# Kernel optimization log

Hardware: AMD Instinct MI355X
Metric: run time of the kernel (lower is better)

The kernel has to match this reference:

```python
import jax, jax.numpy as jnp
import numpy as np

B, T, S = 1, 8, 1024
HID, H = 1152, 16
D = HID // H  # 72
EPS = 1e-6


def rmsnorm(t, gamma):
    # t: [b,t,s,h,d], gamma: [h,d] per-head learnable scale (QKNorm)
    var = jnp.mean(jnp.square(t), axis=-1, keepdims=True)
    return t * jax.lax.rsqrt(var + EPS) * gamma


def setup_inputs() -> dict:
    key = jax.random.key(0)
    ks = jax.random.split(key, 8)
    sc = lambda fan_in: 1.0 / np.sqrt(fan_in)
    x = jax.random.normal(ks[0], (B, T, S, HID), dtype=jnp.float32)
    Wq = jax.random.normal(ks[1], (HID, HID), dtype=jnp.float32) * sc(HID)
    bq = jnp.zeros((HID,), dtype=jnp.float32)
    Wkv = jax.random.normal(ks[2], (HID, 2 * HID), dtype=jnp.float32) * sc(HID)
    bkv = jnp.zeros((2 * HID,), dtype=jnp.float32)
    q_gamma = jnp.ones((H, D), dtype=jnp.float32)
    k_gamma = jnp.ones((H, D), dtype=jnp.float32)
    Wo = jax.random.normal(ks[3], (HID, HID), dtype=jnp.float32) * sc(HID)
    return {"x": x, "Wq": Wq, "bq": bq, "Wkv": Wkv, "bkv": bkv,
            "q_gamma": q_gamma, "k_gamma": k_gamma, "Wo": Wo}


def reference(x, Wq, bq, Wkv, bkv, q_gamma, k_gamma, Wo):
    b, t, s, _ = x.shape
    q = (x @ Wq + bq).reshape(b, t, s, H, D)
    kv = x @ Wkv + bkv
    k, v = jnp.split(kv, 2, axis=-1)
    k = k.reshape(b, t, s, H, D)
    v = v.reshape(b, t, s, H, D)
    q = rmsnorm(q, q_gamma)
    k = rmsnorm(k, k_gamma)
    # NOTE: original applies no 1/sqrt(d) scaling (QKNorm replaces it)
    attn_weight = jnp.einsum('btqhd,btkhd->bthqk', q, k)
    attn = jax.nn.softmax(attn_weight, axis=-1)
    out = jnp.einsum('bthqk,btkhd->btqhd', attn, v).reshape(b, t, s, HID)
    return out @ Wo
```

## Files before the change

### kernel.cpp

```cpp
#include <hip/hip_runtime.h>


typedef __attribute__((ext_vector_type(4))) short s16x4;
typedef __attribute__((ext_vector_type(8))) short s16x8;
typedef __attribute__((ext_vector_type(4))) float f32x4;
typedef __attribute__((ext_vector_type(16))) float f32x16;

__device__ __forceinline__ unsigned short f2b(float x) {
  unsigned u = __float_as_uint(x);
  u += 0x7FFFu + ((u >> 16) & 1u);
  return (unsigned short)(u >> 16);
}
__device__ __forceinline__ float b2f(unsigned short u) {
  return __uint_as_float(((unsigned)u) << 16);
}
__device__ __forceinline__ void gld16(const void* g, void* l) {
  __builtin_amdgcn_global_load_lds(
      (const __attribute__((address_space(1))) void*)g,
      (__attribute__((address_space(3))) void*)l, 16, 0, 0);
}

__global__ __launch_bounds__(256) void cvt_bf16_kernel(const float* __restrict__ in,
                                                       unsigned short* __restrict__ out,
                                                       int n16) {
  int i = blockIdx.x * 256 + threadIdx.x;
  if (i >= n16) return;
  const float4* p = (const float4*)(in + (size_t)i * 16);
  float4 a = p[0], b = p[1], c = p[2], d = p[3];
  s16x8 r0, r1;
  r0[0] = (short)f2b(a.x); r0[1] = (short)f2b(a.y); r0[2] = (short)f2b(a.z); r0[3] = (short)f2b(a.w);
  r0[4] = (short)f2b(c.x); r0[5] = (short)f2b(c.y); r0[6] = (short)f2b(c.z); r0[7] = (short)f2b(c.w);
  r1[0] = (short)f2b(b.x); r1[1] = (short)f2b(b.y); r1[2] = (short)f2b(b.z); r1[3] = (short)f2b(b.w);
  r1[4] = (short)f2b(d.x); r1[5] = (short)f2b(d.y); r1[6] = (short)f2b(d.z); r1[7] = (short)f2b(d.w);
  *(s16x8*)(out + (size_t)i * 16) = r0;
  *(s16x8*)(out + (size_t)i * 16 + 8) = r1;
}

__global__ __launch_bounds__(256) void transpose_cvt_kernel(const float* __restrict__ W,
                                                            unsigned short* __restrict__ WT,
                                                            int K, int N) {
  __shared__ float tile[32][33];
  int n0 = blockIdx.x * 32, k0 = blockIdx.y * 32;
  int tx = threadIdx.x, ty = threadIdx.y;
#pragma unroll
  for (int i = 0; i < 4; i++)
    tile[ty + i * 8][tx] = W[(size_t)(k0 + ty + i * 8) * N + n0 + tx];
  __syncthreads();
  int stx = (tx & 19) | ((tx & 4) << 1) | ((tx & 8) >> 1);
#pragma unroll
  for (int i = 0; i < 4; i++)
    WT[(size_t)(n0 + ty + i * 8) * K + k0 + stx] = f2b(tile[tx][ty + i * 8]);
}

__global__ __launch_bounds__(256) void gemm_qkv_kernel(const unsigned short* __restrict__ A,
                                                       const unsigned short* __restrict__ BT,
                                                       const float* __restrict__ biasq,
                                                       const float* __restrict__ biaskv,
                                                       unsigned short* __restrict__ qn,
                                                       unsigned short* __restrict__ kn,
                                                       unsigned short* __restrict__ vt) {
  constexpr int K = 1152;
  constexpr int NT = K / 32;
  __shared__ __align__(16) unsigned short As[3 * 8192];
  __shared__ __align__(16) unsigned short Bs[3 * 4096];
  int tid = threadIdx.x;
  int lane = tid & 63, wave = tid >> 6;
  int wr = (wave >> 1) * 128, wc = (wave & 1) * 64;
  int l31 = lane & 31, lh = lane >> 5;
  int bid = blockIdx.x;
  int xcd = bid & 7;
  int w = bid >> 3;
  int st = w / 12, inner = w - st * 12;
  int ibx = inner % 3, iby = inner / 3;
  int bx = st * 3 + ibx;
  int by = xcd * 4 + iby;
  int brow = by * 256, bcol = bx * 128;
  const unsigned short* AsrcP[4];
  const unsigned short* BsrcP[2];
  int dstA[4], dstB[2];
#pragma unroll
  for (int i = 0; i < 4; i++) {
    int c = tid + 256 * i;
    int row = c >> 2, j = c & 3;
    AsrcP[i] = A + (size_t)(brow + row) * K + (j ^ ((row >> 1) & 3)) * 8;
    dstA[i] = (wave * 64 + 256 * i) * 8;
  }
#pragma unroll
  for (int i = 0; i < 2; i++) {
    int c = tid + 256 * i;
    int row = c >> 2, j = c & 3;
    BsrcP[i] = BT + (size_t)(bcol + row) * K + (j ^ ((row >> 1) & 3)) * 8;
    dstB[i] = (wave * 64 + 256 * i) * 8;
  }
#define STAGE(KT, BUF)                                           \
  {                                                              \
    int kb = (KT) * 32;                                          \
    gld16(AsrcP[0] + kb, &As[(BUF) * 8192 + dstA[0]]);           \
    gld16(AsrcP[1] + kb, &As[(BUF) * 8192 + dstA[1]]);           \
    gld16(AsrcP[2] + kb, &As[(BUF) * 8192 + dstA[2]]);           \
    gld16(AsrcP[3] + kb, &As[(BUF) * 8192 + dstA[3]]);           \
    gld16(BsrcP[0] + kb, &Bs[(BUF) * 4096 + dstB[0]]);           \
    gld16(BsrcP[1] + kb, &Bs[(BUF) * 4096 + dstB[1]]);           \
  }
  int fr = (l31 >> 1) & 3;
  int slotk[2] = {(lh ^ fr) * 8, ((2 + lh) ^ fr) * 8};
  STAGE(0, 0);
  STAGE(1, 1);
  f32x16 acc[4][2] = {};
  int cur = 0;
  for (int kt = 0; kt < NT; kt++) {
    if (kt < NT - 1)
      asm volatile("s_waitcnt vmcnt(6)\n\ts_barrier" ::: "memory");
    else
      asm volatile("s_waitcnt vmcnt(0)\n\ts_barrier" ::: "memory");
    if (kt + 2 < NT) {
      int nb = (cur == 0) ? 2 : cur - 1;
      STAGE(kt + 2, nb);
    }
    int ab = cur * 8192, bb = cur * 4096;
#pragma unroll
    for (int kk = 0; kk < 2; kk++) {
      int so = slotk[kk];
      s16x8 af[4], bf[2];
#pragma unroll
      for (int m = 0; m < 4; m++)
        af[m] = *(const s16x8*)&As[ab + (wr + m * 32 + l31) * 32 + so];
#pragma unroll
      for (int n = 0; n < 2; n++)
        bf[n] = *(const s16x8*)&Bs[bb + (wc + n * 32 + l31) * 32 + so];
      __builtin_amdgcn_s_setprio(1);
#pragma unroll
      for (int m = 0; m < 4; m++)
#pragma unroll
        for (int n = 0; n < 2; n++)
          acc[m][n] = __builtin_amdgcn_mfma_f32_32x32x16_bf16(af[m], bf[n], acc[m][n], 0, 0, 0);
      __builtin_amdgcn_s_setprio(0);
    }
    cur = (cur == 2) ? 0 : cur + 1;
  }
#undef STAGE
#pragma unroll
  for (int m = 0; m < 4; m++) {
#pragma unroll
    for (int n = 0; n < 2; n++) {
#pragma unroll
      for (int reg = 0; reg < 16; reg++) {
        int grow = brow + wr + m * 32 + (reg & 3) + 8 * (reg >> 2) + 4 * lh;
        int gcol = bcol + wc + n * 32 + l31;
        float v = acc[m][n][reg];
        v += (gcol < 1152) ? biasq[gcol] : biaskv[gcol - 1152];
        int t = grow >> 10, s = grow & 1023;
        if (gcol < 2304) {
          int c = (gcol < 1152) ? gcol : gcol - 1152;
          int h = c / 72, d = c - h * 72;
          unsigned short* dst = (gcol < 1152) ? qn : kn;
          dst[((size_t)((t * 16 + h) * 1024 + s)) * 96 + d] = f2b(v);
        } else {
          int c = gcol - 2304;
          int h = c / 72, d = c - h * 72;
          vt[((size_t)((t * 16 + h) * 80 + d)) * 1024 + s] = f2b(v);
        }
      }
    }
  }
}

__global__ __launch_bounds__(256) void gemm_out_kernel(const unsigned short* __restrict__ A,
                                                       const unsigned short* __restrict__ BT,
                                                       int N, int gx,
                                                       float* __restrict__ outF) {
  constexpr int K = 1152;
  constexpr int NT = K / 32;
  __shared__ __align__(16) unsigned short As[3 * 4096];
  __shared__ __align__(16) unsigned short Bs[3 * 4096];
  int tid = threadIdx.x;
  int lane = tid & 63, wave = tid >> 6;
  int wr = (wave >> 1) * 64, wc = (wave & 1) * 64;
  int l31 = lane & 31, lh = lane >> 5;
  int bid = blockIdx.x;
  int xcd = bid & 7;
  int w = bid >> 3;
  int st = w / 24, inner = w - st * 24;
  int ibx = inner % 3, iby = inner / 3;
  int bx = st * 3 + ibx;
  int by = xcd * 8 + iby;
  int brow = by * 128, bcol = bx * 128;
  const unsigned short* AsrcP[2];
  const unsigned short* BsrcP[2];
  int dst0[2];
#pragma unroll
  for (int i = 0; i < 2; i++) {
    int c = tid + 256 * i;
    int row = c >> 2, j = c & 3;
    int ch = j ^ ((row >> 1) & 3);
    AsrcP[i] = A + (size_t)(brow + row) * K + ch * 8;
    BsrcP[i] = BT + (size_t)(bcol + row) * K + ch * 8;
    dst0[i] = (wave * 64 + 256 * i) * 8;
  }
#define STAGE(KT, BUF)                                          \
  {                                                             \
    int kb = (KT) * 32;                                         \
    gld16(AsrcP[0] + kb, &As[(BUF) * 4096 + dst0[0]]);          \
    gld16(BsrcP[0] + kb, &Bs[(BUF) * 4096 + dst0[0]]);          \
    gld16(AsrcP[1] + kb, &As[(BUF) * 4096 + dst0[1]]);          \
    gld16(BsrcP[1] + kb, &Bs[(BUF) * 4096 + dst0[1]]);          \
  }
  int fr = (l31 >> 1) & 3;
  int slotk[2] = {(lh ^ fr) * 8, ((2 + lh) ^ fr) * 8};
  STAGE(0, 0);
  STAGE(1, 1);
  f32x16 acc[2][2] = {};
  int cur = 0;
  for (int kt = 0; kt < NT; kt++) {
    if (kt < NT - 1)
      asm volatile("s_waitcnt vmcnt(4)\n\ts_barrier" ::: "memory");
    else
      asm volatile("s_waitcnt vmcnt(0)\n\ts_barrier" ::: "memory");
    if (kt + 2 < NT) {
      int nb = (cur == 0) ? 2 : cur - 1;
      STAGE(kt + 2, nb);
    }
    int ab = cur * 4096;
#pragma unroll
    for (int kk = 0; kk < 2; kk++) {
      int so = slotk[kk];
      s16x8 af[2], bf[2];
#pragma unroll
      for (int m = 0; m < 2; m++)
        af[m] = *(const s16x8*)&As[ab + (wr + m * 32 + l31) * 32 + so];
#pragma unroll
      for (int n = 0; n < 2; n++)
        bf[n] = *(const s16x8*)&Bs[ab + (wc + n * 32 + l31) * 32 + so];
      __builtin_amdgcn_s_setprio(1);
#pragma unroll
      for (int m = 0; m < 2; m++)
#pragma unroll
        for (int n = 0; n < 2; n++)
          acc[m][n] = __builtin_amdgcn_mfma_f32_32x32x16_bf16(af[m], bf[n], acc[m][n], 0, 0, 0);
      __builtin_amdgcn_s_setprio(0);
    }
    cur = (cur == 2) ? 0 : cur + 1;
  }
#undef STAGE
#pragma unroll
  for (int m = 0; m < 2; m++) {
#pragma unroll
    for (int n = 0; n < 2; n++) {
#pragma unroll
      for (int reg = 0; reg < 16; reg++) {
        int grow = brow + wr + m * 32 + (reg & 3) + 8 * (reg >> 2) + 4 * lh;
        int gcol = bcol + wc + n * 32 + l31;
        outF[(size_t)grow * N + gcol] = acc[m][n][reg];
      }
    }
  }
}

__global__ __launch_bounds__(256) void rmsnorm2_kernel(unsigned short* __restrict__ qn,
                                                       unsigned short* __restrict__ kn,
                                                       const float* __restrict__ qg,
                                                       const float* __restrict__ kg) {
  int r = blockIdx.x * 4 + (threadIdx.x >> 6);
  int isK = r >= 131072;
  int g = isK ? r - 131072 : r;
  unsigned short* buf = isK ? kn : qn;
  const float* gamma = isK ? kg : qg;
  int h = (g >> 10) & 15;
  size_t base = (size_t)g * 96;
  int l = threadIdx.x & 63;
  float e0 = b2f(buf[base + l]);
  float e1 = 0.f;
  if (l < 8) e1 = b2f(buf[base + 64 + l]);
  float ss = e0 * e0 + e1 * e1;
#pragma unroll
  for (int m = 1; m < 64; m <<= 1) ss += __shfl_xor(ss, m);
  float sc = rsqrtf(ss * (1.0f / 72.0f) + 1e-6f);
  buf[base + l] = f2b(e0 * sc * gamma[h * 72 + l]);
  if (l < 32) {
    float v = 0.f;
    if (l < 8) v = e1 * sc * gamma[h * 72 + 64 + l];
    buf[base + 64 + l] = f2b(v);
  }
}

__global__ __launch_bounds__(256) void attn_kernel(const unsigned short* __restrict__ Qn,
                                                   const unsigned short* __restrict__ Kn,
                                                   const unsigned short* __restrict__ VtG,
                                                   unsigned short* __restrict__ att) {
  __shared__ unsigned short Kl[2][64][100];
  __shared__ unsigned short Vt[2][80][76];
  int tid = threadIdx.x;
  int lane = tid & 63, wave = tid >> 6;
  int l15 = lane & 15, lq = lane >> 4, kf = lq * 4;
  int bid = blockIdx.x;
  int orig = (bid & 7) * 128 + (bid >> 3);
  int qb = orig & 7, th = orig >> 3;
  int t = th >> 4, h = th & 15;
  const unsigned short* Q = Qn + (size_t)th * 1024 * 96;
  const unsigned short* Kp = Kn + (size_t)th * 1024 * 96;
  const unsigned short* Vg = VtG + (size_t)th * 80 * 1024;
  int qrow0 = qb * 128 + wave * 32;
  int krow[3], kco[3], vd[3], vco[3];
#pragma unroll
  for (int i = 0; i < 3; i++) {
    int c = tid + i * 256;
    krow[i] = c / 12;
    kco[i] = c - 12 * krow[i];
    int cc = tid + i * 256;
    vd[i] = cc >> 3;
    vco[i] = cc & 7;
  }
  bool v2 = tid < 128;
  s16x8 sk[3], sv[3];
  s16x8 qf[2][3];
#pragma unroll
  for (int g = 0; g < 2; g++)
#pragma unroll
    for (int c = 0; c < 3; c++) {
      const unsigned short* p = Q + (size_t)(qrow0 + g * 16 + l15) * 96 + c * 32 + kf;
      s16x4 lo = *(const s16x4*)p;
      s16x4 hi = *(const s16x4*)(p + 16);
      qf[g][c] = __builtin_shufflevector(lo, hi, 0, 1, 2, 3, 4, 5, 6, 7);
    }
  f32x4 o[2][5] = {};
  float m_r[2] = {-3.0e38f, -3.0e38f}, l_r[2] = {0.f, 0.f};

#pragma unroll
  for (int i = 0; i < 3; i++)
    sk[i] = *(const s16x8*)(Kp + (size_t)krow[i] * 96 + kco[i] * 8);
#pragma unroll
  for (int i = 0; i < 2; i++)
    sv[i] = *(const s16x8*)(Vg + (size_t)vd[i] * 1024 + vco[i] * 8);
  if (v2) sv[2] = *(const s16x8*)(Vg + (size_t)vd[2] * 1024 + vco[2] * 8);
#pragma unroll
  for (int i = 0; i < 3; i++) *(s16x8*)&Kl[0][krow[i]][kco[i] * 8] = sk[i];
#pragma unroll
  for (int i = 0; i < 2; i++) *(s16x8*)&Vt[0][vd[i]][vco[i] * 8] = sv[i];
  if (v2) *(s16x8*)&Vt[0][vd[2]][vco[2] * 8] = sv[2];

  for (int tt = 0; tt < 16; tt++) {
    __syncthreads();
    int cur = tt & 1;
    if (tt < 15) {
      int kv1 = (tt + 1) * 64;
#pragma unroll
      for (int i = 0; i < 3; i++)
        sk[i] = *(const s16x8*)(Kp + (size_t)(kv1 + krow[i]) * 96 + kco[i] * 8);
#pragma unroll
      for (int i = 0; i < 2; i++)
        sv[i] = *(const s16x8*)(Vg + (size_t)vd[i] * 1024 + kv1 + vco[i] * 8);
      if (v2) sv[2] = *(const s16x8*)(Vg + (size_t)vd[2] * 1024 + kv1 + vco[2] * 8);
    }
#pragma unroll
    for (int g = 0; g < 2; g++) {
      f32x4 st[4];
      __builtin_amdgcn_s_setprio(1);
#pragma unroll
      for (int n = 0; n < 4; n++) {
        f32x4 a = {};
#pragma unroll
        for (int c = 0; c < 3; c++) {
          s16x4 lo = *(const s16x4*)&Kl[cur][n * 16 + l15][c * 32 + kf];
          s16x4 hi = *(const s16x4*)&Kl[cur][n * 16 + l15][c * 32 + kf + 16];
          s16x8 kfr = __builtin_shufflevector(lo, hi, 0, 1, 2, 3, 4, 5, 6, 7);
          a = __builtin_amdgcn_mfma_f32_16x16x32_bf16(kfr, qf[g][c], a, 0, 0, 0);
        }
        st[n] = a;
      }
      __builtin_amdgcn_s_setprio(0);
      float tmax = st[0][0];
#pragma unroll
      for (int n = 0; n < 4; n++)
#pragma unroll
        for (int r = 0; r < 4; r++) tmax = fmaxf(tmax, st[n][r]);
      tmax = fmaxf(tmax, __shfl_xor(tmax, 16));
      tmax = fmaxf(tmax, __shfl_xor(tmax, 32));
      float mn = fmaxf(m_r[g], tmax);
      float scale = __expf(m_r[g] - mn);
      m_r[g] = mn;
      float sum = 0.f;
#pragma unroll
      for (int n = 0; n < 4; n++)
#pragma unroll
        for (int r = 0; r < 4; r++) {
          float p = __expf(st[n][r] - mn);
          st[n][r] = p;
          sum += p;
        }
      sum += __shfl_xor(sum, 16);
      sum += __shfl_xor(sum, 32);
      l_r[g] = l_r[g] * scale + sum;
#pragma unroll
      for (int r = 0; r < 4; r++) {
        float scq = __shfl(scale, 4 * lq + r);
#pragma unroll
        for (int v = 0; v < 5; v++) o[g][v][r] *= scq;
      }
      __builtin_amdgcn_s_setprio(1);
#pragma unroll
      for (int b = 0; b < 2; b++) {
        s16x8 pf;
#pragma unroll
        for (int j = 0; j < 8; j++) pf[j] = (short)f2b(st[2 * b + (j >> 2)][j & 3]);
#pragma unroll
        for (int v = 0; v < 5; v++) {
          s16x4 vlo = *(const s16x4*)&Vt[cur][v * 16 + l15][b * 32 + kf];
          s16x4 vhi = *(const s16x4*)&Vt[cur][v * 16 + l15][b * 32 + kf + 16];
          s16x8 vf = __builtin_shufflevector(vlo, vhi, 0, 1, 2, 3, 4, 5, 6, 7);
          o[g][v] = __builtin_amdgcn_mfma_f32_16x16x32_bf16(pf, vf, o[g][v], 0, 0, 0);
        }
      }
      __builtin_amdgcn_s_setprio(0);
    }
    if (tt < 15) {
      int nxt = cur ^ 1;
#pragma unroll
      for (int i = 0; i < 3; i++) *(s16x8*)&Kl[nxt][krow[i]][kco[i] * 8] = sk[i];
#pragma unroll
      for (int i = 0; i < 2; i++) *(s16x8*)&Vt[nxt][vd[i]][vco[i] * 8] = sv[i];
      if (v2) *(s16x8*)&Vt[nxt][vd[2]][vco[2] * 8] = sv[2];
    }
  }
#pragma unroll
  for (int g = 0; g < 2; g++)
#pragma unroll
    for (int r = 0; r < 4; r++) {
      float inv = 1.0f / __shfl(l_r[g], 4 * lq + r);
      int qrow = qrow0 + g * 16 + 4 * lq + r;
      size_t rowbase = (size_t)(t * 1024 + qrow) * 1152;
#pragma unroll
      for (int v = 0; v < 5; v++) {
        int d = v * 16 + l15;
        if (d < 72) {
          int col = h * 72 + d;
          int scol = (col & ~12) | ((col & 4) << 1) | ((col & 8) >> 1);
          att[rowbase + scol] = f2b(o[g][v][r] * inv);
        }
      }
    }
}

extern "C" void kernel_launch(void* const* d_in, const int* in_sizes, int n_in,
                              void* d_out, int out_size, void* d_ws, size_t ws_size,
                              hipStream_t stream) {
  const float* x   = (const float*)d_in[0];
  const float* Wq  = (const float*)d_in[1];
  const float* bq  = (const float*)d_in[2];
  const float* Wkv = (const float*)d_in[3];
  const float* bkv = (const float*)d_in[4];
  const float* qg  = (const float*)d_in[5];
  const float* kg  = (const float*)d_in[6];
  const float* Wo  = (const float*)d_in[7];
  float* out = (float*)d_out;

  char* w = (char*)d_ws;
  unsigned short* xb   = (unsigned short*)w; w += (size_t)8192 * 1152 * 2;
  unsigned short* WqT  = (unsigned short*)w; w += (size_t)1152 * 1152 * 2;
  unsigned short* WkvT = (unsigned short*)w; w += (size_t)2304 * 1152 * 2;
  unsigned short* WoT  = (unsigned short*)w; w += (size_t)1152 * 1152 * 2;
  unsigned short* qn   = (unsigned short*)w; w += (size_t)128 * 1024 * 96 * 2;
  unsigned short* kn   = (unsigned short*)w; w += (size_t)128 * 1024 * 96 * 2;
  unsigned short* vt   = (unsigned short*)w; w += (size_t)128 * 80 * 1024 * 2;
  unsigned short* att  = (unsigned short*)w; w += (size_t)8192 * 1152 * 2;

  cvt_bf16_kernel<<<2304, 256, 0, stream>>>(x, xb, 9437184 / 16);
  transpose_cvt_kernel<<<dim3(36, 36), dim3(32, 8), 0, stream>>>(Wq, WqT, 1152, 1152);
  transpose_cvt_kernel<<<dim3(72, 36), dim3(32, 8), 0, stream>>>(Wkv, WkvT, 1152, 2304);
  transpose_cvt_kernel<<<dim3(36, 36), dim3(32, 8), 0, stream>>>(Wo, WoT, 1152, 1152);

  gemm_qkv_kernel<<<864, 256, 0, stream>>>(xb, WqT, bq, bkv, qn, kn, vt);
  rmsnorm2_kernel<<<65536, 256, 0, stream>>>(qn, kn, qg, kg);

  attn_kernel<<<1024, 256, 0, stream>>>(qn, kn, vt, att);

  gemm_out_kernel<<<576, 256, 0, stream>>>(att, WoT, 1152, 9, out);
}
```

Measured before the change: 308.8 us.

## Stage V-transpose epilogue through LDS and share K fragments across query groups

In the QKV GEMM, blocks producing V columns now write the biased bf16 tile transposed into shared memory, then emit 16-byte coalesced stores to the transposed V layout instead of scattered 2-byte stores. Bias and head-index math are hoisted out of the per-register loop for Q/K. In attention, the two query groups now share each K fragment read from LDS, issuing both QK MFMAs per load, which halves K LDS reads but keeps both score tiles live and raises register pressure.

```diff
diff --git a/kernel.cpp b/kernel.cpp
--- a/kernel.cpp
+++ b/kernel.cpp
@@ -61,8 +61,9 @@
                                                        unsigned short* __restrict__ vt) {
   constexpr int K = 1152;
   constexpr int NT = K / 32;
-  __shared__ __align__(16) unsigned short As[3 * 8192];
-  __shared__ __align__(16) unsigned short Bs[3 * 4096];
+  __shared__ __align__(16) unsigned short LDSU[3 * 8192 + 3 * 4096];
+  unsigned short* As = LDSU;
+  unsigned short* Bs = LDSU + 3 * 8192;
   int tid = threadIdx.x;
   int lane = tid & 63, wave = tid >> 6;
   int wr = (wave >> 1) * 128, wc = (wave & 1) * 64;
@@ -139,26 +140,49 @@
     cur = (cur == 2) ? 0 : cur + 1;
   }
 #undef STAGE
-#pragma unroll
-  for (int m = 0; m < 4; m++) {
-#pragma unroll
-    for (int n = 0; n < 2; n++) {
-#pragma unroll
-      for (int reg = 0; reg < 16; reg++) {
-        int grow = brow + wr + m * 32 + (reg & 3) + 8 * (reg >> 2) + 4 * lh;
+  if (bcol >= 2304) {
+    __syncthreads();
+    int c0 = bcol - 2304;
+#pragma unroll
+    for (int m = 0; m < 4; m++) {
+#pragma unroll
+      for (int n = 0; n < 2; n++) {
+        int col = wc + n * 32 + l31;
+        float bias = biaskv[1152 + c0 + col];
+#pragma unroll
+        for (int reg = 0; reg < 16; reg++) {
+          int row = wr + m * 32 + (reg & 3) + 8 * (reg >> 2) + 4 * lh;
+          LDSU[col * 264 + row] = f2b(acc[m][n][reg] + bias);
+        }
+      }
+    }
+    __syncthreads();
+    int t = brow >> 10, sbase = brow & 1023;
+#pragma unroll
+    for (int i = 0; i < 16; i++) {
+      int id = tid + 256 * i;
+      int col = id >> 5, rowc = id & 31;
+      int c = c0 + col;
+      int h = c / 72, d = c - h * 72;
+      s16x8 v8 = *(const s16x8*)&LDSU[col * 264 + rowc * 8];
+      *(s16x8*)(vt + ((size_t)((t * 16 + h) * 80 + d)) * 1024 + sbase + rowc * 8) = v8;
+    }
+  } else {
+#pragma unroll
+    for (int m = 0; m < 4; m++) {
+#pragma unroll
+      for (int n = 0; n < 2; n++) {
         int gcol = bcol + wc + n * 32 + l31;
-        float v = acc[m][n][reg];
-        v += (gcol < 1152) ? biasq[gcol] : biaskv[gcol - 1152];
-        int t = grow >> 10, s = grow & 1023;
-        if (gcol < 2304) {
-          int c = (gcol < 1152) ? gcol : gcol - 1152;
-          int h = c / 72, d = c - h * 72;
-          unsigned short* dst = (gcol < 1152) ? qn : kn;
+        float bias = (gcol < 1152) ? biasq[gcol] : biaskv[gcol - 1152];
+        int c = (gcol < 1152) ? gcol : gcol - 1152;
+        int h = c / 72, d = c - h * 72;
+        unsigned short* dst = (gcol < 1152) ? qn : kn;
+#pragma unroll
+        for (int reg = 0; reg < 16; reg++) {
+          int grow = brow + wr + m * 32 + (reg & 3) + 8 * (reg >> 2) + 4 * lh;
+          float v = acc[m][n][reg] + bias;
+          int t = grow >> 10, s = grow & 1023;
           dst[((size_t)((t * 16 + h) * 1024 + s)) * 96 + d] = f2b(v);
-        } else {
-          int c = gcol - 2304;
-          int h = c / 72, d = c - h * 72;
-          vt[((size_t)((t * 16 + h) * 80 + d)) * 1024 + s] = f2b(v);
         }
       }
     }
@@ -312,16 +336,18 @@
   }
   bool v2 = tid < 128;
   s16x8 sk[3], sv[3];
-  s16x8 qf[2][3];
-#pragma unroll
-  for (int g = 0; g < 2; g++)
-#pragma unroll
-    for (int c = 0; c < 3; c++) {
-      const unsigned short* p = Q + (size_t)(qrow0 + g * 16 + l15) * 96 + c * 32 + kf;
-      s16x4 lo = *(const s16x4*)p;
-      s16x4 hi = *(const s16x4*)(p + 16);
-      qf[g][c] = __builtin_shufflevector(lo, hi, 0, 1, 2, 3, 4, 5, 6, 7);
-    }
+  s16x8 qf0[3], qf1[3];
+#pragma unroll
+  for (int c = 0; c < 3; c++) {
+    const unsigned short* p0 = Q + (size_t)(qrow0 + l15) * 96 + c * 32 + kf;
+    s16x4 lo = *(const s16x4*)p0;
+    s16x4 hi = *(const s16x4*)(p0 + 16);
+    qf0[c] = __builtin_shufflevector(lo, hi, 0, 1, 2, 3, 4, 5, 6, 7);
+    const unsigned short* p1 = Q + (size_t)(qrow0 + 16 + l15) * 96 + c * 32 + kf;
+    s16x4 lo1 = *(const s16x4*)p1;
+    s16x4 hi1 = *(const s16x4*)(p1 + 16);
+    qf1[c] = __builtin_shufflevector(lo1, hi1, 0, 1, 2, 3, 4, 5, 6, 7);
+  }
   f32x4 o[2][5] = {};
   float m_r[2] = {-3.0e38f, -3.0e38f}, l_r[2] = {0.f, 0.f};
 
@@ -351,67 +377,71 @@
         sv[i] = *(const s16x8*)(Vg + (size_t)vd[i] * 1024 + kv1 + vco[i] * 8);
       if (v2) sv[2] = *(const s16x8*)(Vg + (size_t)vd[2] * 1024 + kv1 + vco[2] * 8);
     }
-#pragma unroll
-    for (int g = 0; g < 2; g++) {
-      f32x4 st[4];
-      __builtin_amdgcn_s_setprio(1);
-#pragma unroll
-      for (int n = 0; n < 4; n++) {
-        f32x4 a = {};
-#pragma unroll
-        for (int c = 0; c < 3; c++) {
-          s16x4 lo = *(const s16x4*)&Kl[cur][n * 16 + l15][c * 32 + kf];
-          s16x4 hi = *(const s16x4*)&Kl[cur][n * 16 + l15][c * 32 + kf + 16];
-          s16x8 kfr = __builtin_shufflevector(lo, hi, 0, 1, 2, 3, 4, 5, 6, 7);
-          a = __builtin_amdgcn_mfma_f32_16x16x32_bf16(kfr, qf[g][c], a, 0, 0, 0);
-        }
-        st[n] = a;
+    f32x4 st0[4], st1[4];
+    __builtin_amdgcn_s_setprio(1);
+#pragma unroll
+    for (int n = 0; n < 4; n++) {
+      f32x4 a0 = {}, a1 = {};
+#pragma unroll
+      for (int c = 0; c < 3; c++) {
+        s16x4 lo = *(const s16x4*)&Kl[cur][n * 16 + l15][c * 32 + kf];
+        s16x4 hi = *(const s16x4*)&Kl[cur][n * 16 + l15][c * 32 + kf + 16];
+        s16x8 kfr = __builtin_shufflevector(lo, hi, 0, 1, 2, 3, 4, 5, 6, 7);
+        a0 = __builtin_amdgcn_mfma_f32_16x16x32_bf16(kfr, qf0[c], a0, 0, 0, 0);
+        a1 = __builtin_amdgcn_mfma_f32_16x16x32_bf16(kfr, qf1[c], a1, 0, 0, 0);
       }
-      __builtin_amdgcn_s_setprio(0);
-      float tmax = st[0][0];
-#pragma unroll
-      for (int n = 0; n < 4; n++)
-#pragma unroll
-        for (int r = 0; r < 4; r++) tmax = fmaxf(tmax, st[n][r]);
-      tmax = fmaxf(tmax, __shfl_xor(tmax, 16));
-      tmax = fmaxf(tmax, __shfl_xor(tmax, 32));
-      float mn = fmaxf(m_r[g], tmax);
-      float scale = __expf(m_r[g] - mn);
-      m_r[g] = mn;
-      float sum = 0.f;
-#pragma unroll
-      for (int n = 0; n < 4; n++)
-#pragma unroll
-        for (int r = 0; r < 4; r++) {
-          float p = __expf(st[n][r] - mn);
-          st[n][r] = p;
-          sum += p;
-        }
-      sum += __shfl_xor(sum, 16);
-      sum += __shfl_xor(sum, 32);
-      l_r[g] = l_r[g] * scale + sum;
-#pragma unroll
-      for (int r = 0; r < 4; r++) {
-        float scq = __shfl(scale, 4 * lq + r);
-#pragma unroll
-        for (int v = 0; v < 5; v++) o[g][v][r] *= scq;
-      }
-      __builtin_amdgcn_s_setprio(1);
-#pragma unroll
-      for (int b = 0; b < 2; b++) {
-        s16x8 pf;
-#pragma unroll
-        for (int j = 0; j < 8; j++) pf[j] = (short)f2b(st[2 * b + (j >> 2)][j & 3]);
-#pragma unroll
-        for (int v = 0; v < 5; v++) {
-          s16x4 vlo = *(const s16x4*)&Vt[cur][v * 16 + l15][b * 32 + kf];
-          s16x4 vhi = *(const s16x4*)&Vt[cur][v * 16 + l15][b * 32 + kf + 16];
-          s16x8 vf = __builtin_shufflevector(vlo, vhi, 0, 1, 2, 3, 4, 5, 6, 7);
-          o[g][v] = __builtin_amdgcn_mfma_f32_16x16x32_bf16(pf, vf, o[g][v], 0, 0, 0);
-        }
-      }
-      __builtin_amdgcn_s_setprio(0);
-    }
+      st0[n] = a0;
+      st1[n] = a1;
+    }
+    __builtin_amdgcn_s_setprio(0);
+#define SOFTMAX(ST, G)                                                        \
+    {                                                                         \
+      float tmax = ST[0][0];                                                  \
+      _Pragma("unroll") for (int n = 0; n < 4; n++)                           \
+        _Pragma("unroll") for (int r = 0; r < 4; r++)                         \
+          tmax = fmaxf(tmax, ST[n][r]);                                       \
+      tmax = fmaxf(tmax, __shfl_xor(tmax, 16));                               \
+      tmax = fmaxf(tmax, __shfl_xor(tmax, 32));                               \
+      float mn = fmaxf(m_r[G], tmax);                                         \
+      float scale = __expf(m_r[G] - mn);                                      \
+      m_r[G] = mn;                                                            \
+      float sum = 0.f;                                                        \
+      _Pragma("unroll") for (int n = 0; n < 4; n++)                           \
+        _Pragma("unroll") for (int r = 0; r < 4; r++) {                       \
+          float p = __expf(ST[n][r] - mn);                                    \
+          ST[n][r] = p;                                                       \
+          sum += p;                                                           \
+        }                                                                     \
+      sum += __shfl_xor(sum, 16);                                             \
+      sum += __shfl_xor(sum, 32);                                             \
+      l_r[G] = l_r[G] * scale + sum;                                          \
+      _Pragma("unroll") for (int r = 0; r < 4; r++) {                         \
+        float scq = __shfl(scale, 4 * lq + r);                                \
+        _Pragma("unroll") for (int v = 0; v < 5; v++) o[G][v][r] *= scq;      \
+      }                                                                       \
+    }
+#define PV(ST, G)                                                             \
+    {                                                                         \
+      __builtin_amdgcn_s_setprio(1);                                          \
+      _Pragma("unroll") for (int b = 0; b < 2; b++) {                         \
+        s16x8 pf;                                                             \
+        _Pragma("unroll") for (int j = 0; j < 8; j++)                         \
+          pf[j] = (short)f2b(ST[2 * b + (j >> 2)][j & 3]);                    \
+        _Pragma("unroll") for (int v = 0; v < 5; v++) {                       \
+          s16x4 vlo = *(const s16x4*)&Vt[cur][v * 16 + l15][b * 32 + kf];     \
+          s16x4 vhi = *(const s16x4*)&Vt[cur][v * 16 + l15][b * 32 + kf + 16];\
+          s16x8 vf = __builtin_shufflevector(vlo, vhi, 0, 1, 2, 3, 4, 5, 6, 7);\
+          o[G][v] = __builtin_amdgcn_mfma_f32_16x16x32_bf16(pf, vf, o[G][v], 0, 0, 0); \
+        }                                                                     \
+      }                                                                       \
+      __builtin_amdgcn_s_setprio(0);                                          \
+    }
+    SOFTMAX(st0, 0);
+    PV(st0, 0);
+    SOFTMAX(st1, 1);
+    PV(st1, 1);
+#undef SOFTMAX
+#undef PV
     if (tt < 15) {
       int nxt = cur ^ 1;
 #pragma unroll
```

Result: no change. 305.2 us (-1.1%).
